# Performance work log

Hardware: AMD Instinct MI355X
Metric: run time of the kernel (lower is better)

## Reference

```python
import jax, jax.numpy as jnp
import numpy as np

HIDDEN_DIM = 256
CLIP_LEN = 2
B, NQ, T, D = 64, 10, 2048, 256


def setup_inputs() -> dict:
    key = jax.random.key(0)
    ks = jax.random.split(key, 10)
    s = 1.0 / np.sqrt(HIDDEN_DIM)  # torch GRU/Linear init scale
    return {
        "pred_logits": jax.random.normal(ks[0], (B, NQ, 2), jnp.float32),
        "pred_spans": jax.random.uniform(ks[1], (B, NQ, 2), jnp.float32),
        "memory": jax.random.normal(ks[2], (B, T, D), jnp.float32),
        "src_vid": jax.random.normal(ks[3], (B, T, D), jnp.float32),
        "W_ih": jax.random.normal(ks[4], (3 * D, D), jnp.float32) * s,
        "W_hh": jax.random.normal(ks[5], (3 * D, D), jnp.float32) * s,
        "b_ih": jax.random.normal(ks[6], (3 * D,), jnp.float32) * s,
        "b_hh": jax.random.normal(ks[7], (3 * D,), jnp.float32) * s,
        "W_sal": jax.random.normal(ks[8], (D, D), jnp.float32) * s,
        "b_sal": jax.random.normal(ks[9], (D,), jnp.float32) * s,
    }


def _gru_last_hidden(x, W_ih, W_hh, b_ih, b_hh):
    # x: [B, T, D] -> final hidden state [B, D] (torch nn.GRU, h0 = 0)
    b, t, d = x.shape
    gi = jnp.einsum("btd,gd->btg", x, W_ih) + b_ih  # [B, T, 3D], precompute input gates

    def step(h, gi_t):
        gh = jnp.einsum("bd,gd->bg", h, W_hh) + b_hh
        ir, iz, inn = jnp.split(gi_t, 3, axis=-1)
        hr, hz, hn = jnp.split(gh, 3, axis=-1)
        r = jax.nn.sigmoid(ir + hr)
        z = jax.nn.sigmoid(iz + hz)
        n = jnp.tanh(inn + r * hn)
        h_new = (1.0 - z) * n + z * h
        return h_new, None

    h0 = jnp.zeros((b, d), x.dtype)
    hT, _ = jax.lax.scan(step, h0, jnp.swapaxes(gi, 0, 1))
    return hT


def reference(pred_logits, pred_spans, memory, src_vid, W_ih, W_hh, b_ih, b_hh, W_sal, b_sal):
    b, t, d = memory.shape
    # top-1 span selection (sort descending, take first == argmax of class-0 prob)
    scores = jax.nn.softmax(pred_logits, axis=-1)[..., 0]  # [B, NQ]
    best = jnp.argmax(scores, axis=-1)  # [B]
    span = jnp.take_along_axis(pred_spans, best[:, None, None], axis=1)[:, 0, :]  # [B, 2] (cx, w)
    cx, w = span[:, 0], span[:, 1]
    xx = jnp.stack([cx - 0.5 * w, cx + 0.5 * w], axis=-1) * (t * CLIP_LEN)
    se = jnp.floor(xx / CLIP_LEN).astype(jnp.int32)  # [B, 2] start/end frame indices
    start = jnp.clip(se[:, 0], 0, t - 1)
    end_eff = jnp.minimum(se[:, 1], t - 1)
    # on-device dynamic slice + zero pad to fixed length T (replaces python loop)
    idx = start[:, None] + jnp.arange(t)[None, :]  # [B, T]
    valid = idx <= end_eff[:, None]  # empty slice if end < start
    idx_c = jnp.clip(idx, 0, t - 1)
    sliced = jnp.take_along_axis(src_vid, idx_c[..., None], axis=1) * valid[..., None].astype(src_vid.dtype)
    # GRU over padded slice, take last hidden
    hidden = _gru_last_hidden(sliced, W_ih, W_hh, b_ih, b_hh)  # [B, D]
    weight = jnp.einsum("bd,btd->bt", hidden, src_vid)  # [B, T]
    mem = memory * weight[..., None] + memory
    proj = jnp.einsum("btd,ed->bte", mem, W_sal) + b_sal
    saliency = jnp.sum(proj, axis=-1) / np.sqrt(HIDDEN_DIM)
    return saliency  # [B, T]
```

## Files before the change

kernel.cpp:

```cpp
#include <hip/hip_runtime.h>
#include <hip/hip_bf16.h>
#include <stdint.h>

#define T_SEQ 2048
#define DDIM 256
#define G3 768
#define NB 64
#define NQR 10

typedef _Float16 h2f __attribute__((ext_vector_type(2)));

__device__ __forceinline__ float fdot2u(unsigned a, unsigned b, float c) {
    return __builtin_amdgcn_fdot2(__builtin_bit_cast(h2f, a),
                                  __builtin_bit_cast(h2f, b), c, false);
}
__device__ __forceinline__ unsigned packf16(float a, float b) {
    auto p = __builtin_amdgcn_cvt_pkrtz(a, b);
    return __builtin_bit_cast(unsigned, p);
}
__device__ __forceinline__ float sigmf(float x) { return 1.0f / (1.0f + __expf(-x)); }
__device__ __forceinline__ float tanhff(float x) {
    float ax = fabsf(x);
    float e = __expf(2.0f * ax);
    float t = 1.0f - 2.0f / (e + 1.0f);
    return copysignf(t, x);
}

__global__ __launch_bounds__(256) void k_prologue(
    const float* __restrict__ logits, const float* __restrict__ spans,
    const float* __restrict__ W_sal, const float* __restrict__ b_sal,
    int* __restrict__ meta, float* __restrict__ wcol, float* __restrict__ bsum) {
    int tid = threadIdx.x;
    if (tid < NB) {
        int b = tid;
        float bestv = -1e30f; int best = 0;
        for (int q = 0; q < NQR; ++q) {
            float l0 = logits[(b * NQR + q) * 2 + 0];
            float l1 = logits[(b * NQR + q) * 2 + 1];
            float sc = sigmf(l0 - l1);
            if (sc > bestv) { bestv = sc; best = q; }
        }
        float cx = spans[(b * NQR + best) * 2 + 0];
        float w  = spans[(b * NQR + best) * 2 + 1];
        float x0 = (cx - 0.5f * w) * (float)(T_SEQ * 2);
        float x1 = (cx + 0.5f * w) * (float)(T_SEQ * 2);
        int se0 = (int)floorf(x0 * 0.5f);
        int se1 = (int)floorf(x1 * 0.5f);
        int start = min(max(se0, 0), T_SEQ - 1);
        int end_eff = min(se1, T_SEQ - 1);
        int len = end_eff - start + 1;
        if (len < 0) len = 0;
        meta[b] = start; meta[NB + b] = len;
    }
    float acc = 0.f;
    for (int e = 0; e < DDIM; ++e) acc += W_sal[e * DDIM + tid];
    wcol[tid] = acc;
    if (tid < 64) {
        float p = b_sal[tid] + b_sal[tid + 64] + b_sal[tid + 128] + b_sal[tid + 192];
        for (int off = 32; off; off >>= 1) p += __shfl_down(p, off, 64);
        if (tid == 0) *bsum = p;
    }
}

__global__ __launch_bounds__(256) void k_prep(
    const float* __restrict__ W_ih, const float* __restrict__ W_hh,
    float* __restrict__ wt_ih, unsigned* __restrict__ w2t) {
    int g = blockIdx.x, k = threadIdx.x;
    wt_ih[k * G3 + g] = W_ih[g * DDIM + k];
    if (k < 128) {
        float w0 = W_hh[g * DDIM + 2 * k];
        float w1 = W_hh[g * DDIM + 2 * k + 1];
        w2t[k * G3 + g] = packf16(w0, w1);
    }
}

__global__ __launch_bounds__(256) void k_gemm(
    const float* __restrict__ src_vid, const float* __restrict__ wt_ih,
    const float* __restrict__ b_ih, const int* __restrict__ meta,
    float* __restrict__ gi, int t0, int tc, int TC) {
    int b = blockIdx.y;
    int len = meta[NB + b];
    int tb = t0 + blockIdx.x * 16;
    int tcap = t0 + tc; if (tcap > len) tcap = len;
    if (tb >= tcap) return;
    int start = meta[b];
    int j = threadIdx.x;
    int nval = tcap - tb; if (nval > 16) nval = 16;
    float aR[16], aZ[16], aN[16];
    float bR = b_ih[j], bZ = b_ih[DDIM + j], bN = b_ih[2 * DDIM + j];
#pragma unroll
    for (int r = 0; r < 16; ++r) { aR[r] = bR; aZ[r] = bZ; aN[r] = bN; }
    const float* xb = src_vid + ((size_t)b * T_SEQ + start + tb) * DDIM;
    for (int kq = 0; kq < 64; ++kq) {
        float4 xq[16];
#pragma unroll
        for (int r = 0; r < 16; ++r) {
            if (r < nval) xq[r] = *(const float4*)(xb + r * DDIM + kq * 4);
            else          xq[r] = make_float4(0.f, 0.f, 0.f, 0.f);
        }
#pragma unroll
        for (int e = 0; e < 4; ++e) {
            int k = kq * 4 + e;
            float wR = wt_ih[k * G3 + j];
            float wZ = wt_ih[k * G3 + DDIM + j];
            float wN = wt_ih[k * G3 + 2 * DDIM + j];
#pragma unroll
            for (int r = 0; r < 16; ++r) {
                float xv = (e == 0) ? xq[r].x : (e == 1) ? xq[r].y : (e == 2) ? xq[r].z : xq[r].w;
                aR[r] = fmaf(xv, wR, aR[r]);
                aZ[r] = fmaf(xv, wZ, aZ[r]);
                aN[r] = fmaf(xv, wN, aN[r]);
            }
        }
    }
    float* go = gi + ((size_t)b * TC + (tb - t0)) * G3;
    for (int r = 0; r < nval; ++r) {
        go[r * G3 + j] = aR[r];
        go[r * G3 + DDIM + j] = aZ[r];
        go[r * G3 + 2 * DDIM + j] = aN[r];
    }
}

__global__ __launch_bounds__(512, 2) void k_gru(
    const float* __restrict__ gi, const unsigned* __restrict__ w2t,
    const float* __restrict__ b_ih, const float* __restrict__ b_hh,
    const int* __restrict__ meta, float* __restrict__ h_state,
    int t0, int t1, int TC) {
    int b = blockIdx.x;
    int tid = threadIdx.x;
    int c = tid & 255;
    int half = tid >> 8;
    int len = meta[NB + b];

    unsigned wr[64], wz[64], wn[64];
    const unsigned* wbase = w2t + (size_t)(half * 64) * G3;
#pragma unroll
    for (int kk = 0; kk < 64; ++kk) {
        wr[kk] = wbase[kk * G3 + c];
        wz[kk] = wbase[kk * G3 + 256 + c];
        wn[kk] = wbase[kk * G3 + 512 + c];
    }
    float bhR = (half == 0) ? b_hh[c] : 0.f;
    float bhZ = (half == 0) ? b_hh[256 + c] : 0.f;
    float bhN = (half == 0) ? b_hh[512 + c] : 0.f;
    float biR = b_ih[c], biZ = b_ih[256 + c], biN = b_ih[512 + c];

    __shared__ unsigned hl[128];
    __shared__ float pl[3][256];

    float h = 0.f;
    if (t0 != 0 && half == 0) h = h_state[b * DDIM + c];
    if (half == 0) {
        float hp = __shfl_xor(h, 1, 64);
        if (!(c & 1)) hl[c >> 1] = packf16(h, hp);
    }

    const float* gbase = gi + (size_t)b * TC * G3;
    float gR = biR, gZ = biZ, gN = biN;
    if (half == 0 && t0 < len) {
        const float* gp = gbase + c;
        gR = gp[0]; gZ = gp[DDIM]; gN = gp[2 * DDIM];
    }
    __syncthreads();

    for (int t = t0; t < t1; ++t) {
        float nR = biR, nZ = biZ, nN = biN;
        int tn = t + 1;
        if (half == 0 && tn < t1 && tn < len) {
            const float* gp = gbase + (size_t)(tn - t0) * G3 + c;
            nR = gp[0]; nZ = gp[DDIM]; nN = gp[2 * DDIM];
        }
        float r0 = bhR, z0 = bhZ, n0 = bhN, r1 = 0.f, z1 = 0.f, n1 = 0.f;
        const uint4* hb = (const uint4*)(hl + half * 64);
#pragma unroll
        for (int kq = 0; kq < 16; ++kq) {
            uint4 h4 = hb[kq];
            r0 = fdot2u(h4.x, wr[kq * 4 + 0], r0);
            z0 = fdot2u(h4.x, wz[kq * 4 + 0], z0);
            n0 = fdot2u(h4.x, wn[kq * 4 + 0], n0);
            r1 = fdot2u(h4.y, wr[kq * 4 + 1], r1);
            z1 = fdot2u(h4.y, wz[kq * 4 + 1], z1);
            n1 = fdot2u(h4.y, wn[kq * 4 + 1], n1);
            r0 = fdot2u(h4.z, wr[kq * 4 + 2], r0);
            z0 = fdot2u(h4.z, wz[kq * 4 + 2], z0);
            n0 = fdot2u(h4.z, wn[kq * 4 + 2], n0);
            r1 = fdot2u(h4.w, wr[kq * 4 + 3], r1);
            z1 = fdot2u(h4.w, wz[kq * 4 + 3], z1);
            n1 = fdot2u(h4.w, wn[kq * 4 + 3], n1);
        }
        float hr = r0 + r1, hz = z0 + z1, hn = n0 + n1;
        if (half == 1) {
            pl[0][c] = hr; pl[1][c] = hz; pl[2][c] = hn;
        }
        __syncthreads();
        if (half == 0) {
            hr += pl[0][c]; hz += pl[1][c]; hn += pl[2][c];
            float r = sigmf(gR + hr);
            float z = sigmf(gZ + hz);
            float n = tanhff(gN + r * hn);
            h = (1.0f - z) * n + z * h;
            float hp = __shfl_xor(h, 1, 64);
            if (!(c & 1)) hl[c >> 1] = packf16(h, hp);
        }
        gR = nR; gZ = nZ; gN = nN;
        __syncthreads();
    }
    if (half == 0) h_state[b * DDIM + c] = h;
}

__global__ __launch_bounds__(256) void k_epi(
    const float* __restrict__ memory, const float* __restrict__ src_vid,
    const float* __restrict__ h_state, const float* __restrict__ wcol,
    const float* __restrict__ bsum, float* __restrict__ out) {
    int wid = blockIdx.x * 4 + (threadIdx.x >> 6);
    int lane = threadIdx.x & 63;
    int b = wid >> 11;
    int t = wid & 2047;
    const float4* mp = (const float4*)(memory + ((size_t)b * T_SEQ + t) * DDIM);
    const float4* sp = (const float4*)(src_vid + ((size_t)b * T_SEQ + t) * DDIM);
    const float4* hp = (const float4*)(h_state + b * DDIM);
    const float4* wp = (const float4*)wcol;
    float4 m = mp[lane], s = sp[lane], hv = hp[lane], wc = wp[lane];
    float s1 = m.x * wc.x + m.y * wc.y + m.z * wc.z + m.w * wc.w;
    float s2 = hv.x * s.x + hv.y * s.y + hv.z * s.z + hv.w * s.w;
    for (int off = 32; off; off >>= 1) {
        s1 += __shfl_down(s1, off, 64);
        s2 += __shfl_down(s2, off, 64);
    }
    if (lane == 0) out[(size_t)b * T_SEQ + t] = ((1.0f + s2) * s1 + *bsum) * 0.0625f;
}

extern "C" void kernel_launch(void* const* d_in, const int* in_sizes, int n_in,
                              void* d_out, int out_size, void* d_ws, size_t ws_size,
                              hipStream_t stream) {
    const float* logits  = (const float*)d_in[0];
    const float* spans   = (const float*)d_in[1];
    const float* memory  = (const float*)d_in[2];
    const float* src_vid = (const float*)d_in[3];
    const float* W_ih    = (const float*)d_in[4];
    const float* W_hh    = (const float*)d_in[5];
    const float* b_ih    = (const float*)d_in[6];
    const float* b_hh    = (const float*)d_in[7];
    const float* W_sal   = (const float*)d_in[8];
    const float* b_sal   = (const float*)d_in[9];
    float* out = (float*)d_out;
    char* ws = (char*)d_ws;

    const size_t OFF_META = 0;
    const size_t OFF_WCOL = 1024;
    const size_t OFF_BSUM = 2048;
    const size_t OFF_H    = 4096;
    const size_t OFF_W2   = 69632;
    const size_t OFF_WTIH = 462848;
    const size_t OFF_GI   = 1249280;

    int* meta       = (int*)(ws + OFF_META);
    float* wcol     = (float*)(ws + OFF_WCOL);
    float* bsum     = (float*)(ws + OFF_BSUM);
    float* h_state  = (float*)(ws + OFF_H);
    unsigned* w2t   = (unsigned*)(ws + OFF_W2);
    float* wt_ih    = (float*)(ws + OFF_WTIH);
    float* gi       = (float*)(ws + OFF_GI);

    size_t gi_cap = (ws_size > OFF_GI) ? (ws_size - OFF_GI) : 0;
    long long tc_max = (long long)(gi_cap / ((size_t)NB * G3 * 4));
    int TC = (tc_max > T_SEQ) ? T_SEQ : (int)tc_max;
    if (TC < 1) TC = 1;

    k_prologue<<<dim3(1), dim3(256), 0, stream>>>(logits, spans, W_sal, b_sal, meta, wcol, bsum);
    k_prep<<<dim3(G3), dim3(256), 0, stream>>>(W_ih, W_hh, wt_ih, w2t);
    for (int t0 = 0; t0 < T_SEQ; t0 += TC) {
        int tc = T_SEQ - t0; if (tc > TC) tc = TC;
        k_gemm<<<dim3((tc + 15) / 16, NB), dim3(256), 0, stream>>>(
            src_vid, wt_ih, b_ih, meta, gi, t0, tc, TC);
        k_gru<<<dim3(NB), dim3(512), 0, stream>>>(
            gi, w2t, b_ih, b_hh, meta, h_state, t0, t0 + tc, TC);
    }
    k_epi<<<dim3(NB * T_SEQ / 4), dim3(256), 0, stream>>>(
        memory, src_vid, h_state, wcol, bsum, out);
}
```

Baseline: 3.000 ms.

## Use MFMA f16 instructions for GRU recurrent matvec with prepacked weight fragments

Replaces the per-thread fdot2 dot products in the sequential GRU step with 16x16x32 f16 MFMA instructions, splitting the 768 gate outputs across 8 waves with W_hh pre-arranged into register-resident B fragments by a new prep kernel. The hidden state is broadcast as the A operand so only the first output row is used. This aims to shorten the per-timestep latency of the serial recurrence, at the cost of wasting most of the matrix unit throughput and adding a small preprocessing kernel.

```diff
diff --git a/kernel.cpp b/kernel.cpp
--- a/kernel.cpp
+++ b/kernel.cpp
@@ -9,11 +9,10 @@
 #define NQR 10
 
 typedef _Float16 h2f __attribute__((ext_vector_type(2)));
-
-__device__ __forceinline__ float fdot2u(unsigned a, unsigned b, float c) {
-    return __builtin_amdgcn_fdot2(__builtin_bit_cast(h2f, a),
-                                  __builtin_bit_cast(h2f, b), c, false);
-}
+typedef _Float16 f16x8 __attribute__((ext_vector_type(8)));
+typedef float f32x4 __attribute__((ext_vector_type(4)));
+typedef unsigned u32x4 __attribute__((ext_vector_type(4)));
+
 __device__ __forceinline__ unsigned packf16(float a, float b) {
     auto p = __builtin_amdgcn_cvt_pkrtz(a, b);
     return __builtin_bit_cast(unsigned, p);
@@ -63,15 +62,21 @@
 }
 
 __global__ __launch_bounds__(256) void k_prep(
-    const float* __restrict__ W_ih, const float* __restrict__ W_hh,
-    float* __restrict__ wt_ih, unsigned* __restrict__ w2t) {
+    const float* __restrict__ W_ih, float* __restrict__ wt_ih) {
     int g = blockIdx.x, k = threadIdx.x;
     wt_ih[k * G3 + g] = W_ih[g * DDIM + k];
-    if (k < 128) {
-        float w0 = W_hh[g * DDIM + 2 * k];
-        float w1 = W_hh[g * DDIM + 2 * k + 1];
-        w2t[k * G3 + g] = packf16(w0, w1);
-    }
+}
+
+__global__ __launch_bounds__(256) void k_prep2(
+    const float* __restrict__ W_hh, unsigned* __restrict__ wfrag) {
+    int u = blockIdx.x * 256 + threadIdx.x;
+    int jj = u & 3;
+    int l  = (u >> 2) & 63;
+    int kc = (u >> 8) & 7;
+    int wt = u >> 11;
+    int col = wt * 16 + (l & 15);
+    int k = kc * 32 + ((l >> 4) << 3) + jj * 2;
+    wfrag[u] = packf16(W_hh[col * DDIM + k], W_hh[col * DDIM + k + 1]);
 }
 
 __global__ __launch_bounds__(256) void k_gemm(
@@ -121,80 +126,77 @@
     }
 }
 
-__global__ __launch_bounds__(512, 2) void k_gru(
-    const float* __restrict__ gi, const unsigned* __restrict__ w2t,
+__global__ void __launch_bounds__(512)
+__attribute__((amdgpu_waves_per_eu(2, 2))) k_gru(
+    const float* __restrict__ gi, const unsigned* __restrict__ wfrag,
     const float* __restrict__ b_ih, const float* __restrict__ b_hh,
     const int* __restrict__ meta, float* __restrict__ h_state,
     int t0, int t1, int TC) {
-    int b = blockIdx.x;
-    int tid = threadIdx.x;
+    int b = blockIdx.x, tid = threadIdx.x;
+    int lane = tid & 63, w = tid >> 6;
+    int len = meta[NB + b];
+
+    u32x4 bf[48];
+    const u32x4* wfr = (const u32x4*)wfrag;
+#pragma unroll
+    for (int t6 = 0; t6 < 6; ++t6)
+#pragma unroll
+        for (int kc = 0; kc < 8; ++kc)
+            bf[t6 * 8 + kc] = wfr[((w * 6 + t6) * 8 + kc) * 64 + lane];
+
     int c = tid & 255;
-    int half = tid >> 8;
-    int len = meta[NB + b];
-
-    unsigned wr[64], wz[64], wn[64];
-    const unsigned* wbase = w2t + (size_t)(half * 64) * G3;
-#pragma unroll
-    for (int kk = 0; kk < 64; ++kk) {
-        wr[kk] = wbase[kk * G3 + c];
-        wz[kk] = wbase[kk * G3 + 256 + c];
-        wn[kk] = wbase[kk * G3 + 512 + c];
-    }
-    float bhR = (half == 0) ? b_hh[c] : 0.f;
-    float bhZ = (half == 0) ? b_hh[256 + c] : 0.f;
-    float bhN = (half == 0) ? b_hh[512 + c] : 0.f;
     float biR = b_ih[c], biZ = b_ih[256 + c], biN = b_ih[512 + c];
+    float bhR = b_hh[c], bhZ = b_hh[256 + c], bhN = b_hh[512 + c];
 
     __shared__ unsigned hl[128];
-    __shared__ float pl[3][256];
+    __shared__ float pl[768];
 
     float h = 0.f;
-    if (t0 != 0 && half == 0) h = h_state[b * DDIM + c];
-    if (half == 0) {
+    if (tid < 256) {
+        if (t0 != 0) h = h_state[b * DDIM + c];
         float hp = __shfl_xor(h, 1, 64);
         if (!(c & 1)) hl[c >> 1] = packf16(h, hp);
     }
 
     const float* gbase = gi + (size_t)b * TC * G3;
     float gR = biR, gZ = biZ, gN = biN;
-    if (half == 0 && t0 < len) {
+    if (tid < 256 && t0 < t1 && t0 < len) {
         const float* gp = gbase + c;
         gR = gp[0]; gZ = gp[DDIM]; gN = gp[2 * DDIM];
     }
     __syncthreads();
 
+    const f32x4 zf = {0.f, 0.f, 0.f, 0.f};
     for (int t = t0; t < t1; ++t) {
         float nR = biR, nZ = biZ, nN = biN;
         int tn = t + 1;
-        if (half == 0 && tn < t1 && tn < len) {
+        if (tid < 256 && tn < t1 && tn < len) {
             const float* gp = gbase + (size_t)(tn - t0) * G3 + c;
             nR = gp[0]; nZ = gp[DDIM]; nN = gp[2 * DDIM];
         }
-        float r0 = bhR, z0 = bhZ, n0 = bhN, r1 = 0.f, z1 = 0.f, n1 = 0.f;
-        const uint4* hb = (const uint4*)(hl + half * 64);
-#pragma unroll
-        for (int kq = 0; kq < 16; ++kq) {
-            uint4 h4 = hb[kq];
-            r0 = fdot2u(h4.x, wr[kq * 4 + 0], r0);
-            z0 = fdot2u(h4.x, wz[kq * 4 + 0], z0);
-            n0 = fdot2u(h4.x, wn[kq * 4 + 0], n0);
-            r1 = fdot2u(h4.y, wr[kq * 4 + 1], r1);
-            z1 = fdot2u(h4.y, wz[kq * 4 + 1], z1);
-            n1 = fdot2u(h4.y, wn[kq * 4 + 1], n1);
-            r0 = fdot2u(h4.z, wr[kq * 4 + 2], r0);
-            z0 = fdot2u(h4.z, wz[kq * 4 + 2], z0);
-            n0 = fdot2u(h4.z, wn[kq * 4 + 2], n0);
-            r1 = fdot2u(h4.w, wr[kq * 4 + 3], r1);
-            z1 = fdot2u(h4.w, wz[kq * 4 + 3], z1);
-            n1 = fdot2u(h4.w, wn[kq * 4 + 3], n1);
-        }
-        float hr = r0 + r1, hz = z0 + z1, hn = n0 + n1;
-        if (half == 1) {
-            pl[0][c] = hr; pl[1][c] = hz; pl[2][c] = hn;
+        f32x4 cf[6];
+        const u32x4* hb = (const u32x4*)hl;
+#pragma unroll
+        for (int kc = 0; kc < 8; ++kc) {
+            u32x4 av = hb[kc * 4 + (lane >> 4)];
+            f16x8 af = __builtin_bit_cast(f16x8, av);
+#pragma unroll
+            for (int t6 = 0; t6 < 6; ++t6) {
+                cf[t6] = __builtin_amdgcn_mfma_f32_16x16x32_f16(
+                    af, __builtin_bit_cast(f16x8, bf[t6 * 8 + kc]),
+                    (kc == 0) ? zf : cf[t6], 0, 0, 0);
+            }
+        }
+        if (lane < 16) {
+#pragma unroll
+            for (int t6 = 0; t6 < 6; ++t6)
+                pl[(w * 6 + t6) * 16 + lane] = cf[t6][0];
         }
         __syncthreads();
-        if (half == 0) {
-            hr += pl[0][c]; hz += pl[1][c]; hn += pl[2][c];
+        if (tid < 256) {
+            float hr = pl[c] + bhR;
+            float hz = pl[256 + c] + bhZ;
+            float hn = pl[512 + c] + bhN;
             float r = sigmf(gR + hr);
             float z = sigmf(gZ + hz);
             float n = tanhff(gN + r * hn);
@@ -205,7 +207,7 @@
         gR = nR; gZ = nZ; gN = nN;
         __syncthreads();
     }
-    if (half == 0) h_state[b * DDIM + c] = h;
+    if (tid < 256) h_state[b * DDIM + c] = h;
 }
 
 __global__ __launch_bounds__(256) void k_epi(
@@ -250,7 +252,7 @@
     const size_t OFF_WCOL = 1024;
     const size_t OFF_BSUM = 2048;
     const size_t OFF_H    = 4096;
-    const size_t OFF_W2   = 69632;
+    const size_t OFF_FRAG = 69632;
     const size_t OFF_WTIH = 462848;
     const size_t OFF_GI   = 1249280;
 
@@ -258,7 +260,7 @@
     float* wcol     = (float*)(ws + OFF_WCOL);
     float* bsum     = (float*)(ws + OFF_BSUM);
     float* h_state  = (float*)(ws + OFF_H);
-    unsigned* w2t   = (unsigned*)(ws + OFF_W2);
+    unsigned* wfrag = (unsigned*)(ws + OFF_FRAG);
     float* wt_ih    = (float*)(ws + OFF_WTIH);
     float* gi       = (float*)(ws + OFF_GI);
 
@@ -268,13 +270,14 @@
     if (TC < 1) TC = 1;
 
     k_prologue<<<dim3(1), dim3(256), 0, stream>>>(logits, spans, W_sal, b_sal, meta, wcol, bsum);
-    k_prep<<<dim3(G3), dim3(256), 0, stream>>>(W_ih, W_hh, wt_ih, w2t);
+    k_prep<<<dim3(G3), dim3(256), 0, stream>>>(W_ih, wt_ih);
+    k_prep2<<<dim3(384), dim3(256), 0, stream>>>(W_hh, wfrag);
     for (int t0 = 0; t0 < T_SEQ; t0 += TC) {
         int tc = T_SEQ - t0; if (tc > TC) tc = TC;
         k_gemm<<<dim3((tc + 15) / 16, NB), dim3(256), 0, stream>>>(
             src_vid, wt_ih, b_ih, meta, gi, t0, tc, TC);
         k_gru<<<dim3(NB), dim3(512), 0, stream>>>(
-            gi, w2t, b_ih, b_hh, meta, h_state, t0, t0 + tc, TC);
+            gi, wfrag, b_ih, b_hh, meta, h_state, t0, t0 + tc, TC);
     }
     k_epi<<<dim3(NB * T_SEQ / 4), dim3(256), 0, stream>>>(
         memory, src_vid, h_state, wcol, bsum, out);
```

Result: no change. 3.027 ms (+0.9%).

## Store input gates as packed fp16 and vectorize recurrent weight loads

Applied to the files above, without the earlier changes.

The precomputed input-gate buffer is now written as packed fp16 pairs, halving its footprint and read traffic in the sequential GRU loop. This also lets each time chunk cover twice as many steps, so fewer GEMM/GRU launch pairs are needed. The recurrent weights are laid out so each thread loads 128-bit vectors, and inline asm pins them in registers with a waves-per-eu hint to prevent spills or rematerialization. The cost is reduced precision on the input gates and dependence on the compiler honoring the register pinning.

```diff
diff --git a/kernel.cpp b/kernel.cpp
--- a/kernel.cpp
+++ b/kernel.cpp
@@ -9,6 +9,7 @@
 #define NQR 10
 
 typedef _Float16 h2f __attribute__((ext_vector_type(2)));
+typedef unsigned u32x4 __attribute__((ext_vector_type(4)));
 
 __device__ __forceinline__ float fdot2u(unsigned a, unsigned b, float c) {
     return __builtin_amdgcn_fdot2(__builtin_bit_cast(h2f, a),
@@ -17,6 +18,11 @@
 __device__ __forceinline__ unsigned packf16(float a, float b) {
     auto p = __builtin_amdgcn_cvt_pkrtz(a, b);
     return __builtin_bit_cast(unsigned, p);
+}
+__device__ __forceinline__ float unpk(unsigned u, int hi) {
+    unsigned w = hi ? (u >> 16) : u;
+    h2f p = __builtin_bit_cast(h2f, w);
+    return (float)p[0];
 }
 __device__ __forceinline__ float sigmf(float x) { return 1.0f / (1.0f + __expf(-x)); }
 __device__ __forceinline__ float tanhff(float x) {
@@ -25,6 +31,8 @@
     float t = 1.0f - 2.0f / (e + 1.0f);
     return copysignf(t, x);
 }
+
+#define PIN4(x) asm volatile("" : "+v"(x))
 
 __global__ __launch_bounds__(256) void k_prologue(
     const float* __restrict__ logits, const float* __restrict__ spans,
@@ -64,20 +72,19 @@
 
 __global__ __launch_bounds__(256) void k_prep(
     const float* __restrict__ W_ih, const float* __restrict__ W_hh,
-    float* __restrict__ wt_ih, unsigned* __restrict__ w2t) {
+    float* __restrict__ wt_ih, unsigned* __restrict__ w4) {
     int g = blockIdx.x, k = threadIdx.x;
     wt_ih[k * G3 + g] = W_ih[g * DDIM + k];
     if (k < 128) {
-        float w0 = W_hh[g * DDIM + 2 * k];
-        float w1 = W_hh[g * DDIM + 2 * k + 1];
-        w2t[k * G3 + g] = packf16(w0, w1);
+        unsigned v = packf16(W_hh[g * DDIM + 2 * k], W_hh[g * DDIM + 2 * k + 1]);
+        w4[((k >> 2) * G3 + g) * 4 + (k & 3)] = v;
     }
 }
 
 __global__ __launch_bounds__(256) void k_gemm(
     const float* __restrict__ src_vid, const float* __restrict__ wt_ih,
     const float* __restrict__ b_ih, const int* __restrict__ meta,
-    float* __restrict__ gi, int t0, int tc, int TC) {
+    unsigned* __restrict__ gi2, int t0, int tc, int TC) {
     int b = blockIdx.y;
     int len = meta[NB + b];
     int tb = t0 + blockIdx.x * 16;
@@ -113,33 +120,42 @@
             }
         }
     }
-    float* go = gi + ((size_t)b * TC + (tb - t0)) * G3;
+    unsigned* go = gi2 + ((size_t)b * TC + (tb - t0)) * 384;
     for (int r = 0; r < nval; ++r) {
-        go[r * G3 + j] = aR[r];
-        go[r * G3 + DDIM + j] = aZ[r];
-        go[r * G3 + 2 * DDIM + j] = aN[r];
-    }
-}
-
-__global__ __launch_bounds__(512, 2) void k_gru(
-    const float* __restrict__ gi, const unsigned* __restrict__ w2t,
+        float oR = __shfl_xor(aR[r], 1, 64);
+        float oZ = __shfl_xor(aZ[r], 1, 64);
+        float oN = __shfl_xor(aN[r], 1, 64);
+        if (!(j & 1)) {
+            unsigned* gw = go + (size_t)r * 384 + (j >> 1);
+            gw[0]   = packf16(aR[r], oR);
+            gw[128] = packf16(aZ[r], oZ);
+            gw[256] = packf16(aN[r], oN);
+        }
+    }
+}
+
+__global__ void __launch_bounds__(512)
+__attribute__((amdgpu_waves_per_eu(2, 2))) k_gru(
+    const unsigned* __restrict__ gi2, const unsigned* __restrict__ w4,
     const float* __restrict__ b_ih, const float* __restrict__ b_hh,
     const int* __restrict__ meta, float* __restrict__ h_state,
     int t0, int t1, int TC) {
-    int b = blockIdx.x;
-    int tid = threadIdx.x;
-    int c = tid & 255;
-    int half = tid >> 8;
+    int b = blockIdx.x, tid = threadIdx.x;
+    int c = tid & 255, half = tid >> 8;
     int len = meta[NB + b];
 
-    unsigned wr[64], wz[64], wn[64];
-    const unsigned* wbase = w2t + (size_t)(half * 64) * G3;
-#pragma unroll
-    for (int kk = 0; kk < 64; ++kk) {
-        wr[kk] = wbase[kk * G3 + c];
-        wz[kk] = wbase[kk * G3 + 256 + c];
-        wn[kk] = wbase[kk * G3 + 512 + c];
-    }
+    u32x4 wrq[16], wzq[16], wnq[16];
+    const u32x4* w4v = (const u32x4*)w4;
+    const u32x4* wb = w4v + (size_t)(half * 16) * G3;
+#pragma unroll
+    for (int q = 0; q < 16; ++q) {
+        wrq[q] = wb[q * G3 + c];
+        wzq[q] = wb[q * G3 + 256 + c];
+        wnq[q] = wb[q * G3 + 512 + c];
+    }
+#pragma unroll
+    for (int q = 0; q < 16; ++q) { PIN4(wrq[q]); PIN4(wzq[q]); PIN4(wnq[q]); }
+
     float bhR = (half == 0) ? b_hh[c] : 0.f;
     float bhZ = (half == 0) ? b_hh[256 + c] : 0.f;
     float bhN = (half == 0) ? b_hh[512 + c] : 0.f;
@@ -149,17 +165,17 @@
     __shared__ float pl[3][256];
 
     float h = 0.f;
-    if (t0 != 0 && half == 0) h = h_state[b * DDIM + c];
     if (half == 0) {
+        if (t0 != 0) h = h_state[b * DDIM + c];
         float hp = __shfl_xor(h, 1, 64);
         if (!(c & 1)) hl[c >> 1] = packf16(h, hp);
     }
 
-    const float* gbase = gi + (size_t)b * TC * G3;
+    const unsigned* gb2 = gi2 + (size_t)b * TC * 384 + (c >> 1);
+    int sel = c & 1;
     float gR = biR, gZ = biZ, gN = biN;
-    if (half == 0 && t0 < len) {
-        const float* gp = gbase + c;
-        gR = gp[0]; gZ = gp[DDIM]; gN = gp[2 * DDIM];
+    if (half == 0 && t0 < t1 && t0 < len) {
+        gR = unpk(gb2[0], sel); gZ = unpk(gb2[128], sel); gN = unpk(gb2[256], sel);
     }
     __syncthreads();
 
@@ -167,26 +183,28 @@
         float nR = biR, nZ = biZ, nN = biN;
         int tn = t + 1;
         if (half == 0 && tn < t1 && tn < len) {
-            const float* gp = gbase + (size_t)(tn - t0) * G3 + c;
-            nR = gp[0]; nZ = gp[DDIM]; nN = gp[2 * DDIM];
-        }
+            const unsigned* gp = gb2 + (size_t)(tn - t0) * 384;
+            nR = unpk(gp[0], sel); nZ = unpk(gp[128], sel); nN = unpk(gp[256], sel);
+        }
+#pragma unroll
+        for (int q = 0; q < 16; ++q) { PIN4(wrq[q]); PIN4(wzq[q]); PIN4(wnq[q]); }
         float r0 = bhR, z0 = bhZ, n0 = bhN, r1 = 0.f, z1 = 0.f, n1 = 0.f;
-        const uint4* hb = (const uint4*)(hl + half * 64);
-#pragma unroll
-        for (int kq = 0; kq < 16; ++kq) {
-            uint4 h4 = hb[kq];
-            r0 = fdot2u(h4.x, wr[kq * 4 + 0], r0);
-            z0 = fdot2u(h4.x, wz[kq * 4 + 0], z0);
-            n0 = fdot2u(h4.x, wn[kq * 4 + 0], n0);
-            r1 = fdot2u(h4.y, wr[kq * 4 + 1], r1);
-            z1 = fdot2u(h4.y, wz[kq * 4 + 1], z1);
-            n1 = fdot2u(h4.y, wn[kq * 4 + 1], n1);
-            r0 = fdot2u(h4.z, wr[kq * 4 + 2], r0);
-            z0 = fdot2u(h4.z, wz[kq * 4 + 2], z0);
-            n0 = fdot2u(h4.z, wn[kq * 4 + 2], n0);
-            r1 = fdot2u(h4.w, wr[kq * 4 + 3], r1);
-            z1 = fdot2u(h4.w, wz[kq * 4 + 3], z1);
-            n1 = fdot2u(h4.w, wn[kq * 4 + 3], n1);
+        const u32x4* hb = (const u32x4*)hl + half * 16;
+#pragma unroll
+        for (int q = 0; q < 16; ++q) {
+            u32x4 h4 = hb[q];
+            r0 = fdot2u(h4.x, wrq[q].x, r0);
+            z0 = fdot2u(h4.x, wzq[q].x, z0);
+            n0 = fdot2u(h4.x, wnq[q].x, n0);
+            r1 = fdot2u(h4.y, wrq[q].y, r1);
+            z1 = fdot2u(h4.y, wzq[q].y, z1);
+            n1 = fdot2u(h4.y, wnq[q].y, n1);
+            r0 = fdot2u(h4.z, wrq[q].z, r0);
+            z0 = fdot2u(h4.z, wzq[q].z, z0);
+            n0 = fdot2u(h4.z, wnq[q].z, n0);
+            r1 = fdot2u(h4.w, wrq[q].w, r1);
+            z1 = fdot2u(h4.w, wzq[q].w, z1);
+            n1 = fdot2u(h4.w, wnq[q].w, n1);
         }
         float hr = r0 + r1, hz = z0 + z1, hn = n0 + n1;
         if (half == 1) {
@@ -250,7 +268,7 @@
     const size_t OFF_WCOL = 1024;
     const size_t OFF_BSUM = 2048;
     const size_t OFF_H    = 4096;
-    const size_t OFF_W2   = 69632;
+    const size_t OFF_W4   = 69632;
     const size_t OFF_WTIH = 462848;
     const size_t OFF_GI   = 1249280;
 
@@ -258,23 +276,23 @@
     float* wcol     = (float*)(ws + OFF_WCOL);
     float* bsum     = (float*)(ws + OFF_BSUM);
     float* h_state  = (float*)(ws + OFF_H);
-    unsigned* w2t   = (unsigned*)(ws + OFF_W2);
+    unsigned* w4    = (unsigned*)(ws + OFF_W4);
     float* wt_ih    = (float*)(ws + OFF_WTIH);
-    float* gi       = (float*)(ws + OFF_GI);
+    unsigned* gi2   = (unsigned*)(ws + OFF_GI);
 
     size_t gi_cap = (ws_size > OFF_GI) ? (ws_size - OFF_GI) : 0;
-    long long tc_max = (long long)(gi_cap / ((size_t)NB * G3 * 4));
+    long long tc_max = (long long)(gi_cap / ((size_t)NB * 384 * 4));
     int TC = (tc_max > T_SEQ) ? T_SEQ : (int)tc_max;
-    if (TC < 1) TC = 1;
+    if (TC < 16) TC = 16;
 
     k_prologue<<<dim3(1), dim3(256), 0, stream>>>(logits, spans, W_sal, b_sal, meta, wcol, bsum);
-    k_prep<<<dim3(G3), dim3(256), 0, stream>>>(W_ih, W_hh, wt_ih, w2t);
+    k_prep<<<dim3(G3), dim3(256), 0, stream>>>(W_ih, W_hh, wt_ih, w4);
     for (int t0 = 0; t0 < T_SEQ; t0 += TC) {
         int tc = T_SEQ - t0; if (tc > TC) tc = TC;
         k_gemm<<<dim3((tc + 15) / 16, NB), dim3(256), 0, stream>>>(
-            src_vid, wt_ih, b_ih, meta, gi, t0, tc, TC);
+            src_vid, wt_ih, b_ih, meta, gi2, t0, tc, TC);
         k_gru<<<dim3(NB), dim3(512), 0, stream>>>(
-            gi, w2t, b_ih, b_hh, meta, h_state, t0, t0 + tc, TC);
+            gi2, w4, b_ih, b_hh, meta, h_state, t0, t0 + tc, TC);
     }
     k_epi<<<dim3(NB * T_SEQ / 4), dim3(256), 0, stream>>>(
         memory, src_vid, h_state, wcol, bsum, out);
```

Result: no change. 2.993 ms (-0.2%).
